# Kernel optimization log

Measured on AMD Instinct MI355X. Metric: run time of the kernel, lower is better.

Reference implementation:

```python
import jax, jax.numpy as jnp
import numpy as np

G, D, O, L, H, K, B = 33538, 256, 512, 6, 8, 2048, 4
FF = 4 * D
EPS = 1e-5
THRESH = 0.0


def _ln(x, s, b):
    mu = jnp.mean(x, axis=-1, keepdims=True)
    var = jnp.mean((x - mu) ** 2, axis=-1, keepdims=True)
    return (x - mu) * jax.lax.rsqrt(var + EPS) * s + b


def setup_inputs() -> dict:
    key = jax.random.key(0)
    ks = iter(jax.random.split(key, 32))
    s = 0.02
    rn = lambda shape, scale=s: jax.random.normal(next(ks), shape, dtype=jnp.float32) * scale
    inp = {
        'expr': jax.random.normal(next(ks), (B, G), dtype=jnp.float32),
        'gene_emb': rn((G, D)),
        'ep_w1': rn((D, 1), 0.5), 'ep_b1': jnp.zeros((D,), jnp.float32),
        'ep_w2': rn((D, D)), 'ep_b2': jnp.zeros((D,), jnp.float32),
        'cls': rn((D,), 1.0),
        'ln1_s': jnp.ones((L, D), jnp.float32), 'ln1_b': jnp.zeros((L, D), jnp.float32),
        'qkv_w': rn((L, 3 * D, D)), 'qkv_b': jnp.zeros((L, 3 * D), jnp.float32),
        'out_w': rn((L, D, D)), 'out_b': jnp.zeros((L, D), jnp.float32),
        'ln2_s': jnp.ones((L, D), jnp.float32), 'ln2_b': jnp.zeros((L, D), jnp.float32),
        'ff_w1': rn((L, FF, D)), 'ff_b1': jnp.zeros((L, FF), jnp.float32),
        'ff_w2': rn((L, D, FF)), 'ff_b2': jnp.zeros((L, D), jnp.float32),
        'fn_s': jnp.ones((D,), jnp.float32), 'fn_b': jnp.zeros((D,), jnp.float32),
        'pr_w1': rn((O, D)), 'pr_b1': jnp.zeros((O,), jnp.float32),
        'pr_w2': rn((O, O)), 'pr_b2': jnp.zeros((O,), jnp.float32),
    }
    return inp


def _encoder(expr, gene_emb, ep_w1, ep_b1, ep_w2, ep_b2, cls,
             ln1_s, ln1_b, qkv_w, qkv_b, out_w, out_b, ln2_s, ln2_b,
             ff_w1, ff_b1, ff_w2, ff_b2, fn_s, fn_b,
             pr_w1, pr_b1, pr_w2, pr_b2):
    Bb, Gg = expr.shape
    # --- tokeniser: token_i = gene_emb[i] + MLP(expr_i) for all genes ---
    h = jax.nn.gelu(expr[..., None] * ep_w1[:, 0] + ep_b1, approximate=False)  # [B,G,D]
    val_emb = jnp.einsum('bgd,ed->bge', h, ep_w2) + ep_b2
    tokens_all = gene_emb[None] + val_emb  # [B,G,D]
    # active-gene selection: threshold AND top-K
    active = expr > THRESH
    _, topk_idx = jax.lax.top_k(expr, K)
    sel = jnp.zeros((Bb, Gg), bool).at[jnp.arange(Bb)[:, None], topk_idx].set(True)
    active = active & sel
    counts = jnp.sum(active, axis=1)  # [B]
    # vectorized ragged packing: stable sort puts active genes (ascending id) first
    order = jnp.argsort(jnp.logical_not(active), axis=1, stable=True)[:, :K]  # [B,K]
    gathered = jnp.take_along_axis(tokens_all, order[..., None], axis=1)      # [B,K,D]
    valid = jnp.arange(K)[None, :] < counts[:, None]                          # [B,K]
    body = jnp.where(valid[..., None], gathered, 0.0)
    tokens = jnp.concatenate([jnp.broadcast_to(cls, (Bb, 1, D)), body], axis=1)  # [B,T,D]
    mask = jnp.concatenate([jnp.ones((Bb, 1), bool), valid], axis=1)             # [B,T]
    T = K + 1
    dh = D // H
    bias = jnp.where(mask, 0.0, -1e9)[:, None, None, :]  # key padding
    x = tokens
    for i in range(L):
        y = _ln(x, ln1_s[i], ln1_b[i])
        qkv = y @ qkv_w[i].T + qkv_b[i]
        q, k, v = jnp.split(qkv, 3, axis=-1)
        q = q.reshape(Bb, T, H, dh).transpose(0, 2, 1, 3)
        k = k.reshape(Bb, T, H, dh).transpose(0, 2, 1, 3)
        v = v.reshape(Bb, T, H, dh).transpose(0, 2, 1, 3)
        scores = jnp.einsum('bhqd,bhkd->bhqk', q, k) / np.sqrt(dh) + bias
        a = jax.nn.softmax(scores, axis=-1)
        o = jnp.einsum('bhqk,bhkd->bhqd', a, v).transpose(0, 2, 1, 3).reshape(Bb, T, D)
        x = x + o @ out_w[i].T + out_b[i]
        y2 = _ln(x, ln2_s[i], ln2_b[i])
        x = x + jax.nn.gelu(y2 @ ff_w1[i].T + ff_b1[i], approximate=False) @ ff_w2[i].T + ff_b2[i]
    x = _ln(x, fn_s, fn_b)
    cls_out = x[:, 0]
    return jax.nn.gelu(cls_out @ pr_w1.T + pr_b1, approximate=False) @ pr_w2.T + pr_b2


def reference(expr, gene_emb, ep_w1, ep_b1, ep_w2, ep_b2, cls,
              ln1_s, ln1_b, qkv_w, qkv_b, out_w, out_b, ln2_s, ln2_b,
              ff_w1, ff_b1, ff_w2, ff_b2, fn_s, fn_b,
              pr_w1, pr_b1, pr_w2, pr_b2):
    return _encoder(expr, gene_emb, ep_w1, ep_b1, ep_w2, ep_b2, cls,
                    ln1_s, ln1_b, qkv_w, qkv_b, out_w, out_b, ln2_s, ln2_b,
                    ff_w1, ff_b1, ff_w2, ff_b2, fn_s, fn_b,
                    pr_w1, pr_b1, pr_w2, pr_b2)
```

## Files before the change

kernel.cpp:

```cpp
#include <hip/hip_runtime.h>
#include <hip/hip_bf16.h>
#include <math.h>

#define GG 33538
#define DD 256
#define LL 6
#define HH 8
#define KK 2048
#define BB 4
#define TT 2049
#define BT (BB*TT)
#define NT 65
#define TCH 7
#define QSC (0.17677669529663688f * 1.44269504088896340f)

#if __has_builtin(__builtin_amdgcn_exp2f)
#define EXP2(x) __builtin_amdgcn_exp2f(x)
#else
#define EXP2(x) exp2f(x)
#endif
#if __has_builtin(__builtin_amdgcn_rcpf)
#define RCP(x) __builtin_amdgcn_rcpf(x)
#else
#define RCP(x) (1.0f / (x))
#endif

typedef __bf16 bf16x8 __attribute__((ext_vector_type(8)));
typedef float f32x4 __attribute__((ext_vector_type(4)));
typedef float f32x16 __attribute__((ext_vector_type(16)));
typedef unsigned short ub16;

union BW { __bf16 h; ub16 u; };
__device__ __forceinline__ ub16 f2b(float x) { BW w; w.h = (__bf16)x; return w.u; }
__device__ __forceinline__ unsigned pk2(float a, float b) {
    return (unsigned)f2b(a) | ((unsigned)f2b(b) << 16);
}
union U4B { unsigned u[4]; bf16x8 v; };

__device__ __forceinline__ float gelu_f(float x) {
    float ax = fabsf(x) * 0.70710678118654752440f;
    float t = RCP(1.0f + 0.3275911f * ax);
    float p = t * (0.254829592f + t * (-0.284496736f + t * (1.421413741f +
              t * (-1.453152027f + t * 1.061405429f))));
    float e = EXP2(-ax * ax * 1.44269504088896340f);
    float er = 1.0f - p * e;
    float s = (x >= 0.0f) ? er : -er;
    return 0.5f * x * (1.0f + s);
}

__device__ __forceinline__ unsigned to_key(float x) {
    unsigned u = __float_as_uint(x);
    return (u & 0x80000000u) ? ~u : (u | 0x80000000u);
}

__device__ int block_scan_excl_1024(int v, int* shw) {
    int lane = threadIdx.x & 63, w = threadIdx.x >> 6;
    int x = v;
    #pragma unroll
    for (int o = 1; o < 64; o <<= 1) {
        int t = __shfl_up(x, o, 64);
        if (lane >= o) x += t;
    }
    if (lane == 63) shw[w] = x;
    __syncthreads();
    if (w == 0) {
        int y = (lane < 16) ? shw[lane] : 0;
        #pragma unroll
        for (int o = 1; o < 16; o <<= 1) {
            int t = __shfl_up(y, o, 64);
            if (lane >= o) y += t;
        }
        if (lane < 16) shw[lane] = y;
    }
    __syncthreads();
    int off = (w == 0) ? 0 : shw[w - 1];
    return off + x - v;
}

__global__ void topk_init(unsigned* __restrict__ prefwant, unsigned* __restrict__ histg) {
    int i = threadIdx.x;
    if (i < BB * 256) histg[i] = 0u;
    if (i < BB) { prefwant[2 * i] = 0u; prefwant[2 * i + 1] = KK; }
}

__global__ __launch_bounds__(1024) void topk_hist(const float* __restrict__ expr,
                                                  const unsigned* __restrict__ prefwant,
                                                  unsigned* __restrict__ histg, int pass) {
    __shared__ unsigned lh[16][256];
    int b = blockIdx.x, blk = blockIdx.y, tid = threadIdx.x, wv = tid >> 6;
    for (int i = tid; i < 16 * 256; i += 1024) ((unsigned*)lh)[i] = 0u;
    __syncthreads();
    unsigned prefix = prefwant[2 * b];
    int shift = pass * 8;
    unsigned pmask = (pass == 3) ? 0u : (0xFFFFFFFFu << (shift + 8));
    const float* row = expr + (size_t)b * GG;
    int base = blk * 5120;
    #pragma unroll
    for (int j = 0; j < 5; ++j) {
        int g = base + j * 1024 + tid;
        if (g < GG) {
            unsigned key = to_key(row[g]);
            if ((key & pmask) == (prefix & pmask))
                atomicAdd(&lh[wv][(key >> shift) & 255u], 1u);
        }
    }
    __syncthreads();
    if (tid < 256) {
        unsigned s = 0;
        #pragma unroll
        for (int j = 0; j < 16; ++j) s += lh[j][tid];
        if (s) atomicAdd(&histg[b * 256 + tid], s);
    }
}

__global__ void topk_select(unsigned* __restrict__ prefwant,
                            unsigned* __restrict__ histg, int pass) {
    int b = blockIdx.x, lane = threadIdx.x;
    int shift = pass * 8;
    unsigned pref = prefwant[2 * b];
    int want = (int)prefwant[2 * b + 1];
    unsigned cc[4];
    #pragma unroll
    for (int j = 0; j < 4; ++j) cc[j] = histg[b * 256 + lane * 4 + j];
    int s = (int)(cc[0] + cc[1] + cc[2] + cc[3]);
    int incl = s;
    #pragma unroll
    for (int o = 1; o < 64; o <<= 1) { int t = __shfl_up(incl, o); if (lane >= o) incl += t; }
    int total = __shfl(incl, 63);
    int a3 = total - incl;
    int a2 = a3 + (int)cc[3], a1 = a2 + (int)cc[2], a0 = a1 + (int)cc[1];
    int av[4] = {a0, a1, a2, a3};
    #pragma unroll
    for (int j = 0; j < 4; ++j) {
        if (av[j] < want && av[j] + (int)cc[j] >= want) {
            prefwant[2 * b] = pref | ((unsigned)(lane * 4 + j) << shift);
            prefwant[2 * b + 1] = (unsigned)(want - av[j]);
        }
    }
    #pragma unroll
    for (int j = 0; j < 4; ++j) histg[b * 256 + lane * 4 + j] = 0u;
}

__global__ __launch_bounds__(1024) void topk_c1(const float* __restrict__ expr,
                                                const unsigned* __restrict__ prefwant,
                                                int* __restrict__ blkcnt) {
    __shared__ int sred[16][2];
    int b = blockIdx.x, blk = blockIdx.y, tid = threadIdx.x;
    unsigned kth = prefwant[2 * b];
    const float* row = expr + (size_t)b * GG;
    int start = blk * 5120 + tid * 5;
    int eq = 0, gtp = 0;
    #pragma unroll
    for (int j = 0; j < 5; ++j) {
        int g = start + j;
        if (g < GG) {
            float e = row[g];
            unsigned key = to_key(e);
            eq += (key == kth);
            gtp += (key > kth && e > 0.0f);
        }
    }
    #pragma unroll
    for (int o = 1; o < 64; o <<= 1) { eq += __shfl_xor(eq, o); gtp += __shfl_xor(gtp, o); }
    if ((tid & 63) == 0) { sred[tid >> 6][0] = eq; sred[tid >> 6][1] = gtp; }
    __syncthreads();
    if (tid == 0) {
        int te = 0, tg = 0;
        #pragma unroll
        for (int i = 0; i < 16; ++i) { te += sred[i][0]; tg += sred[i][1]; }
        blkcnt[(b * TCH + blk) * 2] = te;
        blkcnt[(b * TCH + blk) * 2 + 1] = tg;
    }
}

__global__ void topk_c2(const unsigned* __restrict__ prefwant,
                        const int* __restrict__ blkcnt,
                        int* __restrict__ blkbase, int* __restrict__ cntout) {
    int b = blockIdx.x, lane = threadIdx.x;
    int eq = 0, gtp = 0;
    if (lane < TCH) {
        eq = blkcnt[(b * TCH + lane) * 2];
        gtp = blkcnt[(b * TCH + lane) * 2 + 1];
    }
    int want = (int)prefwant[2 * b + 1];
    bool kthpos = prefwant[2 * b] > 0x80000000u;
    int incl = eq;
    #pragma unroll
    for (int o = 1; o < 8; o <<= 1) { int t = __shfl_up(incl, o); if (lane >= o) incl += t; }
    int eqb = incl - eq;
    int eqsel = kthpos ? min(max(want - eqb, 0), eq) : 0;
    int act = gtp + eqsel;
    int incl2 = act;
    #pragma unroll
    for (int o = 1; o < 8; o <<= 1) { int t = __shfl_up(incl2, o); if (lane >= o) incl2 += t; }
    int outb = incl2 - act;
    if (lane < TCH) {
        blkbase[(b * TCH + lane) * 2] = eqb;
        blkbase[(b * TCH + lane) * 2 + 1] = outb;
    }
    if (lane == TCH - 1) cntout[b] = incl2;
}

__global__ __launch_bounds__(1024) void topk_c3(const float* __restrict__ expr,
                                                const unsigned* __restrict__ prefwant,
                                                const int* __restrict__ blkbase,
                                                int* __restrict__ idxout) {
    __shared__ int shw[16];
    int b = blockIdx.x, blk = blockIdx.y, tid = threadIdx.x;
    unsigned kth = prefwant[2 * b];
    int want = (int)prefwant[2 * b + 1];
    const float* row = expr + (size_t)b * GG;
    int start = blk * 5120 + tid * 5;
    int eqt = 0;
    #pragma unroll
    for (int j = 0; j < 5; ++j) {
        int g = start + j;
        if (g < GG) eqt += (to_key(row[g]) == kth);
    }
    int eqbase = blkbase[(b * TCH + blk) * 2] + block_scan_excl_1024(eqt, shw);
    __syncthreads();
    int actt = 0;
    {
        int leq = 0;
        #pragma unroll
        for (int j = 0; j < 5; ++j) {
            int g = start + j;
            if (g < GG) {
                float e = row[g];
                unsigned key = to_key(e);
                bool sel = (key > kth) || (key == kth && (eqbase + leq) < want);
                leq += (key == kth);
                actt += (sel && e > 0.0f) ? 1 : 0;
            }
        }
    }
    int pos = blkbase[(b * TCH + blk) * 2 + 1] + block_scan_excl_1024(actt, shw);
    {
        int leq = 0;
        #pragma unroll
        for (int j = 0; j < 5; ++j) {
            int g = start + j;
            if (g < GG) {
                float e = row[g];
                unsigned key = to_key(e);
                bool sel = (key > kth) || (key == kth && (eqbase + leq) < want);
                leq += (key == kth);
                if (sel && e > 0.0f) idxout[b * KK + pos++] = g;
            }
        }
    }
}

__global__ __launch_bounds__(256) void cvt_bf16_kernel(const float* __restrict__ s,
                                                       ub16* __restrict__ d, int n) {
    int i = blockIdx.x * 256 + threadIdx.x;
    if (i < n) d[i] = f2b(s[i]);
}

__global__ __launch_bounds__(256) void build_h_kernel(const float* __restrict__ expr,
                                                      const int* __restrict__ idxb,
                                                      const int* __restrict__ cntb,
                                                      const float* __restrict__ ep_w1,
                                                      const float* __restrict__ ep_b1,
                                                      ub16* __restrict__ H) {
    int i = blockIdx.x * 256 + threadIdx.x;
    int r = i >> 8, d = i & 255;
    int b = r >> 11, jj = r & (KK - 1);
    float v = 0.0f;
    if (jj < cntb[b]) {
        int g = idxb[b * KK + jj];
        float e = expr[(size_t)b * GG + g];
        v = gelu_f(e * ep_w1[d] + ep_b1[d]);
    }
    H[i] = f2b(v);
}

__global__ __launch_bounds__(256) void assemble_kernel(const float* __restrict__ VAL,
                                                       const float* __restrict__ gene_emb,
                                                       const float* __restrict__ clsv,
                                                       const int* __restrict__ idxb,
                                                       const int* __restrict__ cntb,
                                                       float* __restrict__ x) {
    int i = blockIdx.x * 256 + threadIdx.x;
    int r = i >> 8, d = i & 255;
    int b = r / TT, t = r % TT;
    float v;
    if (t == 0) {
        v = clsv[d];
    } else {
        int jj = t - 1;
        if (jj < cntb[b]) {
            int g = idxb[b * KK + jj];
            v = gene_emb[(size_t)g * DD + d] + VAL[((size_t)b * KK + jj) * DD + d];
        } else {
            v = 0.0f;
        }
    }
    x[i] = v;
}

__global__ __launch_bounds__(256) void ln_kernel(const float* __restrict__ X,
                                                 const float* __restrict__ s,
                                                 const float* __restrict__ bsh,
                                                 ub16* __restrict__ Y16,
                                                 float* __restrict__ Yf) {
    int w = threadIdx.x >> 6, lane = threadIdx.x & 63;
    size_t r = (size_t)blockIdx.x * 4 + w;
    float4 xv = *(const float4*)(X + r * 256 + lane * 4);
    float sum = xv.x + xv.y + xv.z + xv.w;
    #pragma unroll
    for (int o = 1; o < 64; o <<= 1) sum += __shfl_xor(sum, o);
    float mu = sum * (1.0f / 256.0f);
    float d0 = xv.x - mu, d1 = xv.y - mu, d2 = xv.z - mu, d3 = xv.w - mu;
    float vs = d0 * d0 + d1 * d1 + d2 * d2 + d3 * d3;
    #pragma unroll
    for (int o = 1; o < 64; o <<= 1) vs += __shfl_xor(vs, o);
    float rstd = rsqrtf(vs * (1.0f / 256.0f) + 1e-5f);
    float4 sc = *(const float4*)(s + lane * 4);
    float4 bc = *(const float4*)(bsh + lane * 4);
    float y0 = d0 * rstd * sc.x + bc.x;
    float y1 = d1 * rstd * sc.y + bc.y;
    float y2 = d2 * rstd * sc.z + bc.z;
    float y3 = d3 * rstd * sc.w + bc.w;
    if (Y16) {
        uint2 o2 = make_uint2(pk2(y0, y1), pk2(y2, y3));
        *(uint2*)(Y16 + r * 256 + lane * 4) = o2;
    } else {
        *(float4*)(Yf + r * 256 + lane * 4) = make_float4(y0, y1, y2, y3);
    }
}

__global__ __launch_bounds__(256) void gemm_bt16(const ub16* __restrict__ A,
                                                 const ub16* __restrict__ W,
                                                 const float* __restrict__ bias,
                                                 const float* __restrict__ R,
                                                 float* __restrict__ Cf,
                                                 ub16* __restrict__ Ch,
                                                 int M, int N, int K, int gelu_flag,
                                                 int qcols) {
    __shared__ ub16 As[2][64][40];
    __shared__ ub16 Ws[2][64][40];
    int tid = threadIdx.x;
    int lane = tid & 63, w = tid >> 6;
    int wr = (w >> 1) * 32, wc = (w & 1) * 32;
    int bm = blockIdx.y * 64, bn = blockIdx.x * 64;
    f32x4 acc[2][2] = {};

    int lrow = tid >> 2, lc8 = (tid & 3) * 8;
    int arow = min(bm + lrow, M - 1);
    const ub16* ap = A + (size_t)arow * K + lc8;
    const ub16* wp = W + (size_t)(bn + lrow) * K + lc8;

    int fr = lane & 15, fc = 8 * (lane >> 4);
    for (int k0 = 0; k0 < K; k0 += 64) {
        bf16x8 av0 = *(const bf16x8*)(ap + k0);
        bf16x8 av1 = *(const bf16x8*)(ap + k0 + 32);
        bf16x8 wv0 = *(const bf16x8*)(wp + k0);
        bf16x8 wv1 = *(const bf16x8*)(wp + k0 + 32);
        *(bf16x8*)&As[0][lrow][lc8] = av0;
        *(bf16x8*)&As[1][lrow][lc8] = av1;
        *(bf16x8*)&Ws[0][lrow][lc8] = wv0;
        *(bf16x8*)&Ws[1][lrow][lc8] = wv1;
        __syncthreads();
        #pragma unroll
        for (int ks = 0; ks < 2; ++ks) {
            bf16x8 a0 = *(const bf16x8*)&As[ks][wr + fr][fc];
            bf16x8 a1 = *(const bf16x8*)&As[ks][wr + 16 + fr][fc];
            bf16x8 b0 = *(const bf16x8*)&Ws[ks][wc + fr][fc];
            bf16x8 b1 = *(const bf16x8*)&Ws[ks][wc + 16 + fr][fc];
            acc[0][0] = __builtin_amdgcn_mfma_f32_16x16x32_bf16(a0, b0, acc[0][0], 0, 0, 0);
            acc[0][1] = __builtin_amdgcn_mfma_f32_16x16x32_bf16(a0, b1, acc[0][1], 0, 0, 0);
            acc[1][0] = __builtin_amdgcn_mfma_f32_16x16x32_bf16(a1, b0, acc[1][0], 0, 0, 0);
            acc[1][1] = __builtin_amdgcn_mfma_f32_16x16x32_bf16(a1, b1, acc[1][1], 0, 0, 0);
        }
        __syncthreads();
    }

    #pragma unroll
    for (int i = 0; i < 2; ++i) {
        #pragma unroll
        for (int j = 0; j < 2; ++j) {
            #pragma unroll
            for (int reg = 0; reg < 4; ++reg) {
                int gm = bm + wr + i * 16 + (lane >> 4) * 4 + reg;
                int gn = bn + wc + j * 16 + (lane & 15);
                if (gm >= M) continue;
                float v = acc[i][j][reg] + bias[gn];
                if (R) v += R[(size_t)gm * N + gn];
                if (gelu_flag) v = gelu_f(v);
                if (gn < qcols) v *= QSC;
                if (Cf) Cf[(size_t)gm * N + gn] = v;
                else    Ch[(size_t)gm * N + gn] = f2b(v);
            }
        }
    }
}

__global__ __launch_bounds__(256) void gemm_bn128(const ub16* __restrict__ A,
                                                  const ub16* __restrict__ W,
                                                  const float* __restrict__ bias,
                                                  ub16* __restrict__ Ch,
                                                  int M, int N, int K, int gelu_flag,
                                                  int qcols) {
    __shared__ ub16 As[2][64][40];
    __shared__ ub16 Ws[2][128][40];
    int tid = threadIdx.x, lane = tid & 63, w = tid >> 6;
    int wr = (w >> 1) * 32, wc = (w & 1) * 64;
    int bm = blockIdx.y * 64, bn = blockIdx.x * 128;
    f32x4 acc[2][4] = {};

    int arow = tid >> 2, aseg = tid & 3, aks = aseg >> 1, aoff = (aseg & 1) * 16;
    const ub16* apg = A + (size_t)min(bm + arow, M - 1) * K + aseg * 16;
    int wrow = tid >> 1, wks = tid & 1;
    const ub16* wpg = W + (size_t)(bn + wrow) * K + wks * 32;
    int fr = lane & 15, fc = 8 * (lane >> 4);

    bf16x8 ra0 = *(const bf16x8*)apg;
    bf16x8 ra1 = *(const bf16x8*)(apg + 8);
    bf16x8 rb0 = *(const bf16x8*)wpg;
    bf16x8 rb1 = *(const bf16x8*)(wpg + 8);
    bf16x8 rb2 = *(const bf16x8*)(wpg + 16);
    bf16x8 rb3 = *(const bf16x8*)(wpg + 24);

    for (int k0 = 0; k0 < K; k0 += 64) {
        *(bf16x8*)&As[aks][arow][aoff] = ra0;
        *(bf16x8*)&As[aks][arow][aoff + 8] = ra1;
        *(bf16x8*)&Ws[wks][wrow][0]  = rb0;
        *(bf16x8*)&Ws[wks][wrow][8]  = rb1;
        *(bf16x8*)&Ws[wks][wrow][16] = rb2;
        *(bf16x8*)&Ws[wks][wrow][24] = rb3;
        __syncthreads();
        if (k0 + 64 < K) {
            ra0 = *(const bf16x8*)(apg + k0 + 64);
            ra1 = *(const bf16x8*)(apg + k0 + 72);
            rb0 = *(const bf16x8*)(wpg + k0 + 64);
            rb1 = *(const bf16x8*)(wpg + k0 + 72);
            rb2 = *(const bf16x8*)(wpg + k0 + 80);
            rb3 = *(const bf16x8*)(wpg + k0 + 88);
        }
        #pragma unroll
        for (int ks = 0; ks < 2; ++ks) {
            bf16x8 af[2], bfv[4];
            #pragma unroll
            for (int mr = 0; mr < 2; ++mr)
                af[mr] = *(const bf16x8*)&As[ks][wr + mr * 16 + fr][fc];
            #pragma unroll
            for (int nr = 0; nr < 4; ++nr)
                bfv[nr] = *(const bf16x8*)&Ws[ks][wc + nr * 16 + fr][fc];
            #pragma unroll
            for (int mr = 0; mr < 2; ++mr)
                #pragma unroll
                for (int nr = 0; nr < 4; ++nr)
                    acc[mr][nr] = __builtin_amdgcn_mfma_f32_16x16x32_bf16(
                        af[mr], bfv[nr], acc[mr][nr], 0, 0, 0);
        }
        __syncthreads();
    }

    #pragma unroll
    for (int mr = 0; mr < 2; ++mr) {
        #pragma unroll
        for (int nr = 0; nr < 4; ++nr) {
            #pragma unroll
            for (int reg = 0; reg < 4; ++reg) {
                int gm = bm + wr + mr * 16 + (lane >> 4) * 4 + reg;
                int gn = bn + wc + nr * 16 + (lane & 15);
                if (gm >= M) continue;
                float v = acc[mr][nr][reg] + bias[gn];
                if (gelu_flag) v = gelu_f(v);
                if (gn < qcols) v *= QSC;
                Ch[(size_t)gm * N + gn] = f2b(v);
            }
        }
    }
}

__global__ __launch_bounds__(256) void kvprep(const ub16* __restrict__ qkv,
                                              ub16* __restrict__ Kc,
                                              ub16* __restrict__ Vt) {
    __shared__ unsigned vl[32][33];
    int bh = blockIdx.x, b = bh >> 3, h = bh & 7;
    int c = blockIdx.y;
    int tid = threadIdx.x;
    int krel = tid >> 2;
    int key = c * 64 + krel;
    int d8 = (tid & 3) * 8;
    U4B kv = {}, vv = {};
    if (key < TT) {
        const ub16* p = qkv + ((size_t)(b * TT + key)) * 768 + 256 + h * 32 + d8;
        kv.v = *(const bf16x8*)p;
        vv.v = *(const bf16x8*)(p + 256);
    }
    int kt = c * 2 + (krel >> 5);
    if (kt < NT)
        *(bf16x8*)(Kc + (((size_t)bh * NT + kt) * 32 + (krel & 31)) * 32 + d8) = kv.v;

    unsigned pu[4];
    #pragma unroll
    for (int j = 0; j < 4; ++j) pu[j] = __shfl_xor(vv.u[j], 4);
    if (!(krel & 1)) {
        int kp = krel >> 1;
        #pragma unroll
        for (int j = 0; j < 8; ++j) {
            unsigned mine = (vv.u[j >> 1] >> ((j & 1) * 16)) & 0xffffu;
            unsigned oth  = (pu[j >> 1] >> ((j & 1) * 16)) & 0xffffu;
            vl[d8 + j][kp] = mine | (oth << 16);
        }
    }
    __syncthreads();
    int d = tid >> 3, c8 = tid & 7;
    int kt2 = c * 2 + (c8 >> 2);
    if (kt2 < NT) {
        unsigned* vdst = (unsigned*)(Vt + (((size_t)bh * NT + kt2) * 32 + d) * 32);
        #pragma unroll
        for (int ih = 0; ih < 2; ++ih) {
            int pkr = (c8 & 3) * 4 + ih * 2;
            int dp = (pkr & 1) | ((pkr & 2) << 1) | ((pkr & 4) >> 1) | (pkr & 8);
            uint2 o2 = make_uint2(vl[d][c8 * 4 + ih * 2], vl[d][c8 * 4 + ih * 2 + 1]);
            *(uint2*)(vdst + dp) = o2;
        }
    }
}

__global__ __launch_bounds__(256) void attn_mfma7(const ub16* __restrict__ qkv,
                                                  const ub16* __restrict__ Kc,
                                                  const ub16* __restrict__ Vt,
                                                  const int* __restrict__ cnt,
                                                  ub16* __restrict__ attno) {
    __shared__ float Olds[4][32][33];
    __shared__ float Oll[4][32];
    int bh = blockIdx.x, b = bh >> 3, h = bh & 7;
    int tid = threadIdx.x;
    int w = tid >> 6, lane = tid & 63, hi = lane >> 5, q = lane & 31;
    int qt = blockIdx.y;
    int t = qt * 32 + q;
    int nvalid = cnt[b] + 1;
    int nkt = (nvalid + 31) >> 5;
    int nfull = (nvalid & 31) ? nkt - 1 : nkt;

    int tc = min(t, TT - 1);
    const ub16* qp = qkv + ((size_t)(b * TT + tc)) * 768 + h * 32 + 8 * hi;
    bf16x8 bq0 = *(const bf16x8*)qp;
    bf16x8 bq1 = *(const bf16x8*)(qp + 16);

    float l = 0.0f;
    f32x16 ot = {};

    const ub16* kbase = Kc + (size_t)bh * NT * 1024 + q * 32 + 8 * hi;
    const ub16* vbase = Vt + (size_t)bh * NT * 1024 + q * 32 + 8 * hi;

    size_t cur = (size_t)min(w, NT - 1) * 1024;
    bf16x8 ka0 = *(const bf16x8*)(kbase + cur);
    bf16x8 ka1 = *(const bf16x8*)(kbase + cur + 16);
    bf16x8 va0 = *(const bf16x8*)(vbase + cur);
    bf16x8 va1 = *(const bf16x8*)(vbase + cur + 16);

    for (int kt = w; kt < nkt; kt += 4) {
        size_t nxt = (size_t)min(kt + 4, NT - 1) * 1024;
        bf16x8 nk0 = *(const bf16x8*)(kbase + nxt);
        bf16x8 nk1 = *(const bf16x8*)(kbase + nxt + 16);
        bf16x8 nv0 = *(const bf16x8*)(vbase + nxt);
        bf16x8 nv1 = *(const bf16x8*)(vbase + nxt + 16);

        f32x16 z = {};
        f32x16 st = __builtin_amdgcn_mfma_f32_32x32x16_bf16(ka0, bq0, z, 0, 0, 0);
        st = __builtin_amdgcn_mfma_f32_32x32x16_bf16(ka1, bq1, st, 0, 0, 0);

        if (kt >= nfull) {
            int lim = nvalid - (kt << 5);
            #pragma unroll
            for (int r = 0; r < 16; ++r) {
                int off = (r & 3) + 8 * (r >> 2) + 4 * hi;
                if (off >= lim) st[r] = -1e30f;
            }
        }

        float p[16];
        #pragma unroll
        for (int r = 0; r < 16; ++r) p[r] = EXP2(st[r]);
        float s0 = (p[0] + p[1]) + (p[2] + p[3]);
        float s1 = (p[4] + p[5]) + (p[6] + p[7]);
        float s2 = (p[8] + p[9]) + (p[10] + p[11]);
        float s3 = (p[12] + p[13]) + (p[14] + p[15]);
        l += (s0 + s1) + (s2 + s3);

        bf16x8 pv0, pv1;
        #pragma unroll
        for (int jj = 0; jj < 8; ++jj) {
            pv0[jj] = (__bf16)p[jj];
            pv1[jj] = (__bf16)p[8 + jj];
        }
        ot = __builtin_amdgcn_mfma_f32_32x32x16_bf16(va0, pv0, ot, 0, 0, 0);
        ot = __builtin_amdgcn_mfma_f32_32x32x16_bf16(va1, pv1, ot, 0, 0, 0);

        ka0 = nk0; ka1 = nk1; va0 = nv0; va1 = nv1;
    }

    l += __shfl_xor(l, 32);
    #pragma unroll
    for (int r = 0; r < 16; ++r) {
        int d = (r & 3) + 8 * (r >> 2) + 4 * hi;
        Olds[w][q][d] = ot[r];
    }
    if (hi == 0) Oll[w][q] = l;
    __syncthreads();

    int qq = tid >> 3, dg = tid & 7;
    int trow = qt * 32 + qq;
    if (trow < TT) {
        float L = Oll[0][qq] + Oll[1][qq] + Oll[2][qq] + Oll[3][qq];
        float rL = 1.0f / L;
        float o[4];
        #pragma unroll
        for (int j = 0; j < 4; ++j) {
            int d = dg * 4 + j;
            o[j] = (Olds[0][qq][d] + Olds[1][qq][d] +
                    Olds[2][qq][d] + Olds[3][qq][d]) * rL;
        }
        uint2 o2 = make_uint2(pk2(o[0], o[1]), pk2(o[2], o[3]));
        *(uint2*)(attno + ((size_t)(b * TT + trow)) * 256 + h * 32 + dg * 4) = o2;
    }
}

__global__ __launch_bounds__(256) void head1_kernel(const float* __restrict__ Y,
                                                    const float* __restrict__ w1,
                                                    const float* __restrict__ b1,
                                                    float* __restrict__ t1) {
    int b = blockIdx.x, w = threadIdx.x >> 6, lane = threadIdx.x & 63;
    int o = blockIdx.y * 4 + w;
    float4 c = *(const float4*)(Y + ((size_t)b * TT) * DD + lane * 4);
    float4 ww = *(const float4*)(w1 + (size_t)o * 256 + lane * 4);
    float s = c.x * ww.x + c.y * ww.y + c.z * ww.z + c.w * ww.w;
    #pragma unroll
    for (int off = 1; off < 64; off <<= 1) s += __shfl_xor(s, off);
    if (lane == 0) t1[b * 512 + o] = gelu_f(s + b1[o]);
}

__global__ __launch_bounds__(256) void head2_kernel(const float* __restrict__ t1,
                                                    const float* __restrict__ w2,
                                                    const float* __restrict__ b2,
                                                    float* __restrict__ out) {
    int b = blockIdx.x, w = threadIdx.x >> 6, lane = threadIdx.x & 63;
    int o = blockIdx.y * 4 + w;
    const float* tp = t1 + b * 512 + lane * 8;
    const float* wp = w2 + (size_t)o * 512 + lane * 8;
    float4 a0 = *(const float4*)tp;
    float4 a1 = *(const float4*)(tp + 4);
    float4 b0 = *(const float4*)wp;
    float4 b1v = *(const float4*)(wp + 4);
    float s = a0.x * b0.x + a0.y * b0.y + a0.z * b0.z + a0.w * b0.w +
              a1.x * b1v.x + a1.y * b1v.y + a1.z * b1v.z + a1.w * b1v.w;
    #pragma unroll
    for (int off = 1; off < 64; off <<= 1) s += __shfl_xor(s, off);
    if (lane == 0) out[b * 512 + o] = s + b2[o];
}

extern "C" void kernel_launch(void* const* d_in, const int* in_sizes, int n_in,
                              void* d_out, int out_size, void* d_ws, size_t ws_size,
                              hipStream_t stream) {
    (void)in_sizes; (void)n_in; (void)out_size; (void)ws_size;
    const float* expr     = (const float*)d_in[0];
    const float* gene_emb = (const float*)d_in[1];
    const float* ep_w1    = (const float*)d_in[2];
    const float* ep_b1    = (const float*)d_in[3];
    const float* ep_w2    = (const float*)d_in[4];
    const float* ep_b2    = (const float*)d_in[5];
    const float* clsv     = (const float*)d_in[6];
    const float* ln1_s    = (const float*)d_in[7];
    const float* ln1_b    = (const float*)d_in[8];
    const float* qkv_w    = (const float*)d_in[9];
    const float* qkv_b    = (const float*)d_in[10];
    const float* out_w    = (const float*)d_in[11];
    const float* out_b    = (const float*)d_in[12];
    const float* ln2_s    = (const float*)d_in[13];
    const float* ln2_b    = (const float*)d_in[14];
    const float* ff_w1    = (const float*)d_in[15];
    const float* ff_b1    = (const float*)d_in[16];
    const float* ff_w2    = (const float*)d_in[17];
    const float* ff_b2    = (const float*)d_in[18];
    const float* fn_s     = (const float*)d_in[19];
    const float* fn_b     = (const float*)d_in[20];
    const float* pr_w1    = (const float*)d_in[21];
    const float* pr_b1    = (const float*)d_in[22];
    const float* pr_w2    = (const float*)d_in[23];
    const float* pr_b2    = (const float*)d_in[24];
    float* outp = (float*)d_out;

    const size_t KVSZ = (size_t)32 * NT * 1024;

    float* x   = (float*)d_ws;
    float* VAL = x + (size_t)BT * 256;
    ub16* y16   = (ub16*)(VAL + (size_t)8192 * 256);
    ub16* qkv16 = y16 + (size_t)BT * 256;
    ub16* att16 = qkv16 + (size_t)BT * 768;
    ub16* ff116 = att16 + (size_t)BT * 256;
    ub16* kc_h  = ff116 + (size_t)BT * 1024;
    ub16* wqkv  = kc_h + KVSZ;
    ub16* wout  = wqkv + (size_t)LL * 768 * 256;
    ub16* wff1  = wout + (size_t)LL * 256 * 256;
    ub16* wff2  = wff1 + (size_t)LL * 1024 * 256;
    ub16* wep2  = wff2 + (size_t)LL * 256 * 1024;
    int*  idxb  = (int*)(wep2 + (size_t)256 * 256);
    int*  cntb  = idxb + BB * KK;
    unsigned* prefwant = (unsigned*)(cntb + BB);
    unsigned* histg    = prefwant + BB * 2;
    int* blkcnt  = (int*)(histg + BB * 256);
    int* blkbase = blkcnt + BB * TCH * 2;
    float* t1f   = (float*)(blkbase + BB * TCH * 2);
    ub16* H16 = kc_h;
    ub16* Kc  = kc_h;
    ub16* Vt  = (ub16*)VAL;

    topk_init<<<1, 1024, 0, stream>>>(prefwant, histg);
    for (int p = 3; p >= 0; --p) {
        topk_hist<<<dim3(BB, TCH), 1024, 0, stream>>>(expr, prefwant, histg, p);
        topk_select<<<BB, 64, 0, stream>>>(prefwant, histg, p);
    }
    topk_c1<<<dim3(BB, TCH), 1024, 0, stream>>>(expr, prefwant, blkcnt);
    topk_c2<<<BB, 64, 0, stream>>>(prefwant, blkcnt, blkbase, cntb);
    topk_c3<<<dim3(BB, TCH), 1024, 0, stream>>>(expr, prefwant, blkbase, idxb);

    cvt_bf16_kernel<<<(LL*768*256 + 255)/256, 256, 0, stream>>>(qkv_w, wqkv, LL*768*256);
    cvt_bf16_kernel<<<(LL*256*256 + 255)/256, 256, 0, stream>>>(out_w, wout, LL*256*256);
    cvt_bf16_kernel<<<(LL*1024*256 + 255)/256, 256, 0, stream>>>(ff_w1, wff1, LL*1024*256);
    cvt_bf16_kernel<<<(LL*256*1024 + 255)/256, 256, 0, stream>>>(ff_w2, wff2, LL*256*1024);
    cvt_bf16_kernel<<<(256*256 + 255)/256, 256, 0, stream>>>(ep_w2, wep2, 256*256);

    build_h_kernel<<<(BB * KK * DD) / 256, 256, 0, stream>>>(expr, idxb, cntb, ep_w1, ep_b1, H16);
    gemm_bt16<<<dim3(4, 128), 256, 0, stream>>>(H16, wep2, ep_b2, nullptr, VAL, nullptr,
                                                8192, 256, 256, 0, 0);
    assemble_kernel<<<BT, 256, 0, stream>>>(VAL, gene_emb, clsv, idxb, cntb, x);

    for (int i = 0; i < LL; ++i) {
        ln_kernel<<<BT / 4, 256, 0, stream>>>(x, ln1_s + i * DD, ln1_b + i * DD, y16, nullptr);
        gemm_bn128<<<dim3(6, 129), 256, 0, stream>>>(y16, wqkv + (size_t)i * 768 * 256,
                                                     qkv_b + i * 768, qkv16,
                                                     BT, 768, 256, 0, 256);
        kvprep<<<dim3(BB * HH, 33), 256, 0, stream>>>(qkv16, Kc, Vt);
        attn_mfma7<<<dim3(BB * HH, NT), 256, 0, stream>>>(qkv16, Kc, Vt, cntb, att16);
        gemm_bt16<<<dim3(4, 129), 256, 0, stream>>>(att16, wout + (size_t)i * 256 * 256,
                                                    out_b + i * 256, x, x, nullptr,
                                                    BT, 256, 256, 0, 0);
        ln_kernel<<<BT / 4, 256, 0, stream>>>(x, ln2_s + i * DD, ln2_b + i * DD, y16, nullptr);
        gemm_bn128<<<dim3(8, 129), 256, 0, stream>>>(y16, wff1 + (size_t)i * 1024 * 256,
                                                     ff_b1 + i * 1024, ff116,
                                                     BT, 1024, 256, 1, 0);
        gemm_bt16<<<dim3(4, 129), 256, 0, stream>>>(ff116, wff2 + (size_t)i * 256 * 1024,
                                                    ff_b2 + i * 256, x, x, nullptr,
                                                    BT, 256, 1024, 0, 0);
    }

    ln_kernel<<<BT / 4, 256, 0, stream>>>(x, fn_s, fn_b, nullptr, VAL);
    head1_kernel<<<dim3(BB, 128), 256, 0, stream>>>(VAL, pr_w1, pr_b1, t1f);
    head2_kernel<<<dim3(BB, 128), 256, 0, stream>>>(t1f, pr_w2, pr_b2, outp);
}
```

Baseline: 825.3 us.

## Fuse K/V attention-layout scatter into QKV GEMM epilogue, drop kvprep kernel

```diff
diff --git a/kernel.cpp b/kernel.cpp
--- a/kernel.cpp
+++ b/kernel.cpp
@@ -299,6 +299,17 @@
     x[i] = v;
 }
 
+__global__ __launch_bounds__(256) void kvtail_zero(ub16* __restrict__ Kc,
+                                                   ub16* __restrict__ Vt) {
+    int bh = blockIdx.x;
+    size_t base = ((size_t)bh * NT + (NT - 1)) * 1024;
+    for (int i = threadIdx.x; i < 992; i += 256) {
+        int key = 1 + (i >> 5), d = i & 31;
+        Kc[base + key * 32 + d] = 0;
+        Vt[base + d * 32 + key] = 0;
+    }
+}
+
 __global__ __launch_bounds__(256) void ln_kernel(const float* __restrict__ X,
                                                  const float* __restrict__ s,
                                                  const float* __restrict__ bsh,
@@ -400,8 +411,9 @@
                                                   const ub16* __restrict__ W,
                                                   const float* __restrict__ bias,
                                                   ub16* __restrict__ Ch,
-                                                  int M, int N, int K, int gelu_flag,
-                                                  int qcols) {
+                                                  ub16* __restrict__ Kc,
+                                                  ub16* __restrict__ Vt,
+                                                  int M, int N, int K, int gelu_flag) {
     __shared__ ub16 As[2][64][40];
     __shared__ ub16 Ws[2][128][40];
     int tid = threadIdx.x, lane = tid & 63, w = tid >> 6;
@@ -468,56 +480,25 @@
                 if (gm >= M) continue;
                 float v = acc[mr][nr][reg] + bias[gn];
                 if (gelu_flag) v = gelu_f(v);
-                if (gn < qcols) v *= QSC;
-                Ch[(size_t)gm * N + gn] = f2b(v);
+                if (!Kc) {
+                    Ch[(size_t)gm * N + gn] = f2b(v);
+                } else {
+                    int b = gm / TT, t = gm - b * TT;
+                    if (gn < 256) {
+                        Ch[(size_t)gm * 768 + gn] = f2b(v * QSC);
+                    } else if (gn < 512) {
+                        int h = (gn - 256) >> 5, d = (gn - 256) & 31;
+                        int bh = b * 8 + h;
+                        Kc[(((size_t)bh * NT + (t >> 5)) * 32 + (t & 31)) * 32 + d] = f2b(v);
+                    } else {
+                        int h = (gn - 512) >> 5, d = (gn - 512) & 31;
+                        int bh = b * 8 + h;
+                        int tt = t & 31;
+                        int pos = (tt & 3) | ((tt & 4) << 1) | ((tt & 8) >> 1) | (tt & 16);
+                        Vt[(((size_t)bh * NT + (t >> 5)) * 32 + d) * 32 + pos] = f2b(v);
+                    }
+                }
             }
-        }
-    }
-}
-
-__global__ __launch_bounds__(256) void kvprep(const ub16* __restrict__ qkv,
-                                              ub16* __restrict__ Kc,
-                                              ub16* __restrict__ Vt) {
-    __shared__ unsigned vl[32][33];
-    int bh = blockIdx.x, b = bh >> 3, h = bh & 7;
-    int c = blockIdx.y;
-    int tid = threadIdx.x;
-    int krel = tid >> 2;
-    int key = c * 64 + krel;
-    int d8 = (tid & 3) * 8;
-    U4B kv = {}, vv = {};
-    if (key < TT) {
-        const ub16* p = qkv + ((size_t)(b * TT + key)) * 768 + 256 + h * 32 + d8;
-        kv.v = *(const bf16x8*)p;
-        vv.v = *(const bf16x8*)(p + 256);
-    }
-    int kt = c * 2 + (krel >> 5);
-    if (kt < NT)
-        *(bf16x8*)(Kc + (((size_t)bh * NT + kt) * 32 + (krel & 31)) * 32 + d8) = kv.v;
-
-    unsigned pu[4];
-    #pragma unroll
-    for (int j = 0; j < 4; ++j) pu[j] = __shfl_xor(vv.u[j], 4);
-    if (!(krel & 1)) {
-        int kp = krel >> 1;
-        #pragma unroll
-        for (int j = 0; j < 8; ++j) {
-            unsigned mine = (vv.u[j >> 1] >> ((j & 1) * 16)) & 0xffffu;
-            unsigned oth  = (pu[j >> 1] >> ((j & 1) * 16)) & 0xffffu;
-            vl[d8 + j][kp] = mine | (oth << 16);
-        }
-    }
-    __syncthreads();
-    int d = tid >> 3, c8 = tid & 7;
-    int kt2 = c * 2 + (c8 >> 2);
-    if (kt2 < NT) {
-        unsigned* vdst = (unsigned*)(Vt + (((size_t)bh * NT + kt2) * 32 + d) * 32);
-        #pragma unroll
-        for (int ih = 0; ih < 2; ++ih) {
-            int pkr = (c8 & 3) * 4 + ih * 2;
-            int dp = (pkr & 1) | ((pkr & 2) << 1) | ((pkr & 4) >> 1) | (pkr & 8);
-            uint2 o2 = make_uint2(vl[d][c8 * 4 + ih * 2], vl[d][c8 * 4 + ih * 2 + 1]);
-            *(uint2*)(vdst + dp) = o2;
         }
     }
 }
@@ -730,21 +711,21 @@
     gemm_bt16<<<dim3(4, 128), 256, 0, stream>>>(H16, wep2, ep_b2, nullptr, VAL, nullptr,
                                                 8192, 256, 256, 0, 0);
     assemble_kernel<<<BT, 256, 0, stream>>>(VAL, gene_emb, clsv, idxb, cntb, x);
+    kvtail_zero<<<32, 256, 0, stream>>>(Kc, Vt);
 
     for (int i = 0; i < LL; ++i) {
         ln_kernel<<<BT / 4, 256, 0, stream>>>(x, ln1_s + i * DD, ln1_b + i * DD, y16, nullptr);
         gemm_bn128<<<dim3(6, 129), 256, 0, stream>>>(y16, wqkv + (size_t)i * 768 * 256,
-                                                     qkv_b + i * 768, qkv16,
-                                                     BT, 768, 256, 0, 256);
-        kvprep<<<dim3(BB * HH, 33), 256, 0, stream>>>(qkv16, Kc, Vt);
+                                                     qkv_b + i * 768, qkv16, Kc, Vt,
+                                                     BT, 768, 256, 0);
         attn_mfma7<<<dim3(BB * HH, NT), 256, 0, stream>>>(qkv16, Kc, Vt, cntb, att16);
         gemm_bt16<<<dim3(4, 129), 256, 0, stream>>>(att16, wout + (size_t)i * 256 * 256,
                                                     out_b + i * 256, x, x, nullptr,
                                                     BT, 256, 256, 0, 0);
         ln_kernel<<<BT / 4, 256, 0, stream>>>(x, ln2_s + i * DD, ln2_b + i * DD, y16, nullptr);
         gemm_bn128<<<dim3(8, 129), 256, 0, stream>>>(y16, wff1 + (size_t)i * 1024 * 256,
-                                                     ff_b1 + i * 1024, ff116,
-                                                     BT, 1024, 256, 1, 0);
+                                                     ff_b1 + i * 1024, ff116, nullptr, nullptr,
+                                                     BT, 1024, 256, 1);
         gemm_bt16<<<dim3(4, 129), 256, 0, stream>>>(ff116, wff2 + (size_t)i * 256 * 1024,
                                                     ff_b2 + i * 256, x, x, nullptr,
                                                     BT, 256, 1024, 0, 0);
```

Result: no change. 826.2 us (+0.1%).
